# Optimization experiments

Hardware: AMD Instinct MI355X
Metric: run time of the kernel (lower is better)

## Reference

```python
import jax, jax.numpy as jnp
import numpy as np

N_NODES = 50000
N_EDGES = 800000
IN_FEATS, H_FEATS, N_CLASSES = 64, 64, 16


def setup_inputs() -> dict:
    key = jax.random.key(0)
    ks = jax.random.split(key, 8)
    x = jax.random.normal(ks[0], (N_NODES, IN_FEATS), dtype=jnp.float32)
    src = jax.random.randint(ks[1], (N_EDGES,), 0, N_NODES, dtype=jnp.int64)
    dst = jax.random.randint(ks[2], (N_EDGES,), 0, N_NODES, dtype=jnp.int64)
    W_self1 = jax.random.normal(ks[3], (IN_FEATS, H_FEATS), dtype=jnp.float32) / np.sqrt(IN_FEATS)
    W_neigh1 = jax.random.normal(ks[4], (IN_FEATS, H_FEATS), dtype=jnp.float32) / np.sqrt(IN_FEATS)
    b1 = jnp.zeros((H_FEATS,), dtype=jnp.float32)
    W_self2 = jax.random.normal(ks[5], (H_FEATS, N_CLASSES), dtype=jnp.float32) / np.sqrt(H_FEATS)
    W_neigh2 = jax.random.normal(ks[6], (H_FEATS, N_CLASSES), dtype=jnp.float32) / np.sqrt(H_FEATS)
    b2 = jnp.zeros((N_CLASSES,), dtype=jnp.float32)
    return {"x": x, "src": src, "dst": dst,
            "W_self1": W_self1, "W_neigh1": W_neigh1, "b1": b1,
            "W_self2": W_self2, "W_neigh2": W_neigh2, "b2": b2}


def _mean_agg(h, src, dst, n_nodes):
    # gather source-node features along edges, sum into destinations, divide by in-degree
    summed = jax.ops.segment_sum(h[src], dst, num_segments=n_nodes)  # [N, d]
    deg = jax.ops.segment_sum(jnp.ones_like(src, dtype=h.dtype), dst, num_segments=n_nodes)
    return summed / jnp.maximum(deg, 1.0)[:, None]  # zero in-degree -> zeros (DGL semantics)


def _sage_layer(h, src, dst, W_self, W_neigh, b):
    h_neigh = _mean_agg(h, src, dst, h.shape[0])
    return h @ W_self + h_neigh @ W_neigh + b


def reference(x, src, dst, W_self1, W_neigh1, b1, W_self2, W_neigh2, b2):
    h = _sage_layer(x, src, dst, W_self1, W_neigh1, b1)
    h = jax.nn.relu(h)
    out = _sage_layer(h, src, dst, W_self2, W_neigh2, b2)
    return out
```

## Files before the change

### kernel.cpp

```cpp
#include <hip/hip_runtime.h>
#include <hip/hip_bf16.h>
#include <cstring>


#define FEATS 64
#define CLS   16
#define ESCAT 8
#define CAPN  64

typedef unsigned short bf16_t;
typedef float floatx2 __attribute__((ext_vector_type(2)));

__device__ __forceinline__ float bfbits2f(unsigned lo16) {
    unsigned v = lo16 << 16;
    float f;
    __builtin_memcpy(&f, &v, 4);
    return f;
}
__device__ __forceinline__ bf16_t f2bf(float f) {
    unsigned u;
    __builtin_memcpy(&u, &f, 4);
    u = (u + 0x7FFFu + ((u >> 16) & 1u)) >> 16;
    return (bf16_t)u;
}
__device__ __forceinline__ unsigned pack2(float a, float b) {
    return (unsigned)f2bf(a) | ((unsigned)f2bf(b) << 16);
}
__device__ __forceinline__ unsigned pack4_fp8(float a, float b, float c, float d) {
    int q = __builtin_amdgcn_cvt_pk_fp8_f32(a, b, 0, false);
    q = __builtin_amdgcn_cvt_pk_fp8_f32(c, d, q, true);
    return (unsigned)q;
}

__global__ __launch_bounds__(256) void fused_pg_kernel(
    const int* __restrict__ src, const int* __restrict__ dst,
    int* __restrict__ cnt, int* __restrict__ csr, int E,
    const float* __restrict__ x, const float* __restrict__ Ws,
    const float* __restrict__ Wn, bf16_t* __restrict__ selfo,
    unsigned char* __restrict__ t1, int N, int nbp)
{
    __shared__ float smem[16512];
    int t = threadIdx.x;

    if ((int)blockIdx.x < nbp) {
        int e0 = (blockIdx.x * 256 + t) * ESCAT;
#pragma unroll
        for (int h = 0; h < ESCAT / 4; ++h) {
            int e = e0 + h * 4;
            if (e < E) {
                int4 sv = *(const int4*)(src + e);
                int4 dv = *(const int4*)(dst + e);
                int slot;
                slot = atomicAdd(&cnt[dv.x], 1);
                if (slot < CAPN) csr[(size_t)dv.x * CAPN + slot] = sv.x;
                slot = atomicAdd(&cnt[dv.y], 1);
                if (slot < CAPN) csr[(size_t)dv.y * CAPN + slot] = sv.y;
                slot = atomicAdd(&cnt[dv.z], 1);
                if (slot < CAPN) csr[(size_t)dv.z * CAPN + slot] = sv.z;
                slot = atomicAdd(&cnt[dv.w], 1);
                if (slot < CAPN) csr[(size_t)dv.w * CAPN + slot] = sv.w;
            }
        }
        return;
    }

    float* Wc = smem;
    float* xs = smem + 8192;
    int node0 = ((int)blockIdx.x - nbp) * 128;

    for (int idx = t; idx < 64 * 128; idx += 256) {
        int k = idx >> 7, c = idx & 127;
        Wc[idx] = (c < 64) ? Ws[k * 64 + c] : Wn[k * 64 + (c - 64)];
    }
    for (int idx = t; idx < 128 * 16; idx += 256) {
        int row = idx >> 4, c4 = idx & 15;
        int node = node0 + row;
        float4 v = (node < N) ? ((const float4*)(x + (size_t)node * 64))[c4]
                              : make_float4(0.f, 0.f, 0.f, 0.f);
        float* p = &xs[row * 65 + c4 * 4];
        p[0] = v.x; p[1] = v.y; p[2] = v.z; p[3] = v.w;
    }
    __syncthreads();

    int m = t & 31;
    int g = t >> 5;
    float acc[4][16];
#pragma unroll
    for (int j = 0; j < 4; ++j)
#pragma unroll
        for (int c = 0; c < 16; ++c) acc[j][c] = 0.f;

    for (int k = 0; k < 64; ++k) {
        float w[16];
        const float* wp = &Wc[k * 128 + g * 16];
#pragma unroll
        for (int c = 0; c < 16; ++c) w[c] = wp[c];
        float a0 = xs[m * 65 + k];
        float a1 = xs[(m + 32) * 65 + k];
        float a2 = xs[(m + 64) * 65 + k];
        float a3 = xs[(m + 96) * 65 + k];
#pragma unroll
        for (int c = 0; c < 16; ++c) {
            acc[0][c] += a0 * w[c];
            acc[1][c] += a1 * w[c];
            acc[2][c] += a2 * w[c];
            acc[3][c] += a3 * w[c];
        }
    }
#pragma unroll
    for (int j = 0; j < 4; ++j) {
        int node = node0 + m + 32 * j;
        if (node < N) {
            if (g < 4) {
                bf16_t* dstp = selfo + (size_t)node * 64 + g * 16;
                uint4 p0, p1;
                p0.x = pack2(acc[j][0],  acc[j][1]);  p0.y = pack2(acc[j][2],  acc[j][3]);
                p0.z = pack2(acc[j][4],  acc[j][5]);  p0.w = pack2(acc[j][6],  acc[j][7]);
                p1.x = pack2(acc[j][8],  acc[j][9]);  p1.y = pack2(acc[j][10], acc[j][11]);
                p1.z = pack2(acc[j][12], acc[j][13]); p1.w = pack2(acc[j][14], acc[j][15]);
                *(uint4*)(dstp) = p0;
                *(uint4*)(dstp + 8) = p1;
            } else {
                unsigned char* dstp = t1 + (size_t)node * 64 + (g - 4) * 16;
                uint4 q;
                q.x = pack4_fp8(acc[j][0],  acc[j][1],  acc[j][2],  acc[j][3]);
                q.y = pack4_fp8(acc[j][4],  acc[j][5],  acc[j][6],  acc[j][7]);
                q.z = pack4_fp8(acc[j][8],  acc[j][9],  acc[j][10], acc[j][11]);
                q.w = pack4_fp8(acc[j][12], acc[j][13], acc[j][14], acc[j][15]);
                *(uint4*)(dstp) = q;
            }
        }
    }
}

__global__ __launch_bounds__(256) void gather64_kernel(
    const int* __restrict__ csr, const int* __restrict__ cnt,
    const unsigned char* __restrict__ t1, const bf16_t* __restrict__ selfo,
    bf16_t* __restrict__ h1, const float* __restrict__ b1, int N)
{
    int wid = (blockIdx.x * 256 + threadIdx.x) >> 6;
    int lane = threadIdx.x & 63;
    int eslot = lane >> 4;
    int cg = lane & 15;
    if (wid >= N) return;
    int eraw = csr[(size_t)wid * CAPN + lane];
    int d = cnt[wid];
    size_t o = (size_t)wid * 64 + cg * 4;
    uint2 su;
    float4 bb;
    if (eslot == 0) {
        su = *(const uint2*)(selfo + o);
        bb = *(const float4*)(b1 + cg * 4);
    }
    d = min(d, CAPN);
    float ax = 0.f, ay = 0.f, az = 0.f, aw = 0.f;
    if (d > 0) {
        int dm1 = d - 1;
#define G64_ACC(r, m)                                                      \
        {                                                                  \
            floatx2 p_ = __builtin_amdgcn_cvt_pk_f32_fp8((int)(r), false); \
            floatx2 q_ = __builtin_amdgcn_cvt_pk_f32_fp8((int)(r), true);  \
            ax += (m) * p_.x; ay += (m) * p_.y;                            \
            az += (m) * q_.x; aw += (m) * q_.y;                            \
        }
#define G64_BATCH(K0, KN)                                                  \
        {                                                                  \
            int ss[KN - K0];                                               \
            float mk[KN - K0];                                             \
            unsigned rr[KN - K0];                                          \
            _Pragma("unroll")                                              \
            for (int k = K0; k < KN; ++k) {                                \
                int i = eslot + 4 * k;                                     \
                int idx = i > dm1 ? dm1 : i;                               \
                mk[k - K0] = (i <= dm1) ? 1.f : 0.f;                       \
                ss[k - K0] = __shfl(eraw, idx);                            \
            }                                                              \
            _Pragma("unroll")                                              \
            for (int k = 0; k < KN - K0; ++k)                              \
                rr[k] = *(const unsigned*)(t1 + (size_t)ss[k] * 64 + cg * 4); \
            _Pragma("unroll")                                              \
            for (int k = 0; k < KN - K0; ++k) G64_ACC(rr[k], mk[k]);       \
        }
        if (d <= 16) {
            G64_BATCH(0, 4)
        } else if (d <= 32) {
            G64_BATCH(0, 8)
        } else {
            G64_BATCH(0, 16)
        }
#undef G64_BATCH
#undef G64_ACC
        ax += __shfl_xor(ax, 16); ay += __shfl_xor(ay, 16);
        az += __shfl_xor(az, 16); aw += __shfl_xor(aw, 16);
        ax += __shfl_xor(ax, 32); ay += __shfl_xor(ay, 32);
        az += __shfl_xor(az, 32); aw += __shfl_xor(aw, 32);
    }
    if (eslot == 0) {
        float inv = 1.f / fmaxf((float)d, 1.f);
        float rx = fmaxf(bfbits2f(su.x & 0xffff) + ax * inv + bb.x, 0.f);
        float ry = fmaxf(bfbits2f(su.x >> 16)    + ay * inv + bb.y, 0.f);
        float rz = fmaxf(bfbits2f(su.y & 0xffff) + az * inv + bb.z, 0.f);
        float rw = fmaxf(bfbits2f(su.y >> 16)    + aw * inv + bb.w, 0.f);
        uint2 pk;
        pk.x = pack2(rx, ry);
        pk.y = pack2(rz, rw);
        *(uint2*)(h1 + o) = pk;
    }
}

__global__ __launch_bounds__(256) void gather16_kernel(
    const int* __restrict__ csr, const int* __restrict__ cnt,
    const bf16_t* __restrict__ t2,
    float* __restrict__ outp, const float* __restrict__ b2, int N)
{
    int wid = (blockIdx.x * 256 + threadIdx.x) >> 6;
    int lane = threadIdx.x & 63;
    int eslot = lane >> 3;
    int c2 = lane & 7;
    if (wid >= N) return;
    int eraw = csr[(size_t)wid * CAPN + lane];
    int d = cnt[wid];
    size_t o = (size_t)wid * 16 + c2 * 2;
    float2 oo = make_float2(0.f, 0.f), bbv = make_float2(0.f, 0.f);
    if (eslot == 0) {
        oo = *(const float2*)(outp + o);
        bbv = *(const float2*)(b2 + c2 * 2);
    }
    d = min(d, CAPN);
    float a0 = 0.f, a1 = 0.f;
    if (d > 0) {
        int dm1 = d - 1;
#define G16_BATCH(KN)                                                      \
        {                                                                  \
            int ss[KN];                                                    \
            float mk[KN];                                                  \
            unsigned uu[KN];                                               \
            _Pragma("unroll")                                              \
            for (int k = 0; k < KN; ++k) {                                 \
                int i = eslot + 8 * k;                                     \
                int idx = i > dm1 ? dm1 : i;                               \
                mk[k] = (i <= dm1) ? 1.f : 0.f;                            \
                ss[k] = __shfl(eraw, idx);                                 \
            }                                                              \
            _Pragma("unroll")                                              \
            for (int k = 0; k < KN; ++k)                                   \
                uu[k] = *(const unsigned*)(t2 + (size_t)ss[k] * 16 + c2 * 2); \
            _Pragma("unroll")                                              \
            for (int k = 0; k < KN; ++k) {                                 \
                a0 += mk[k] * bfbits2f(uu[k] & 0xffff);                    \
                a1 += mk[k] * bfbits2f(uu[k] >> 16);                       \
            }                                                              \
        }
        if (d <= 16) {
            G16_BATCH(2)
        } else if (d <= 32) {
            G16_BATCH(4)
        } else {
            G16_BATCH(8)
        }
#undef G16_BATCH
        a0 += __shfl_xor(a0, 8);  a1 += __shfl_xor(a1, 8);
        a0 += __shfl_xor(a0, 16); a1 += __shfl_xor(a1, 16);
        a0 += __shfl_xor(a0, 32); a1 += __shfl_xor(a1, 32);
    }
    if (eslot == 0) {
        float inv = 1.f / fmaxf((float)d, 1.f);
        float2 r;
        r.x = oo.x + a0 * inv + bbv.x;
        r.y = oo.y + a1 * inv + bbv.y;
        *(float2*)(outp + o) = r;
    }
}

__global__ __launch_bounds__(256) void gemm2_kernel(
    const bf16_t* __restrict__ h1, const float* __restrict__ Ws,
    const float* __restrict__ Wn, float* __restrict__ outp,
    bf16_t* __restrict__ t2, int N)
{
    __shared__ float Wc[64 * 32];
    __shared__ float xs[128 * 65];
    int t = threadIdx.x;
    int node0 = blockIdx.x * 128;

    for (int idx = t; idx < 64 * 32; idx += 256) {
        int k = idx >> 5, c = idx & 31;
        Wc[idx] = (c < 16) ? Ws[k * 16 + c] : Wn[k * 16 + (c - 16)];
    }
    for (int idx = t; idx < 128 * 8; idx += 256) {
        int row = idx >> 3, c8 = idx & 7;
        int node = node0 + row;
        float* p = &xs[row * 65 + c8 * 8];
        if (node < N) {
            uint4 u = *(const uint4*)(h1 + (size_t)node * 64 + c8 * 8);
            p[0] = bfbits2f(u.x & 0xffff); p[1] = bfbits2f(u.x >> 16);
            p[2] = bfbits2f(u.y & 0xffff); p[3] = bfbits2f(u.y >> 16);
            p[4] = bfbits2f(u.z & 0xffff); p[5] = bfbits2f(u.z >> 16);
            p[6] = bfbits2f(u.w & 0xffff); p[7] = bfbits2f(u.w >> 16);
        } else {
            for (int qq = 0; qq < 8; ++qq) p[qq] = 0.f;
        }
    }
    __syncthreads();

    int m = t & 31;
    int g = t >> 5;
    float acc[4][4];
#pragma unroll
    for (int j = 0; j < 4; ++j)
#pragma unroll
        for (int c = 0; c < 4; ++c) acc[j][c] = 0.f;

    for (int k = 0; k < 64; ++k) {
        float w[4];
        const float* wp = &Wc[k * 32 + g * 4];
#pragma unroll
        for (int c = 0; c < 4; ++c) w[c] = wp[c];
        float a0 = xs[m * 65 + k];
        float a1 = xs[(m + 32) * 65 + k];
        float a2 = xs[(m + 64) * 65 + k];
        float a3 = xs[(m + 96) * 65 + k];
#pragma unroll
        for (int c = 0; c < 4; ++c) {
            acc[0][c] += a0 * w[c];
            acc[1][c] += a1 * w[c];
            acc[2][c] += a2 * w[c];
            acc[3][c] += a3 * w[c];
        }
    }
#pragma unroll
    for (int j = 0; j < 4; ++j) {
        int node = node0 + m + 32 * j;
        if (node < N) {
            if (g < 4) {
                *(float4*)(outp + (size_t)node * 16 + g * 4) =
                    make_float4(acc[j][0], acc[j][1], acc[j][2], acc[j][3]);
            } else {
                uint2 pk;
                pk.x = pack2(acc[j][0], acc[j][1]);
                pk.y = pack2(acc[j][2], acc[j][3]);
                *(uint2*)(t2 + (size_t)node * 16 + (g - 4) * 4) = pk;
            }
        }
    }
}

extern "C" void kernel_launch(void* const* d_in, const int* in_sizes, int n_in,
                              void* d_out, int out_size, void* d_ws, size_t ws_size,
                              hipStream_t stream) {
    const float* x   = (const float*)d_in[0];
    const int*   src = (const int*)d_in[1];
    const int*   dst = (const int*)d_in[2];
    const float* Ws1 = (const float*)d_in[3];
    const float* Wn1 = (const float*)d_in[4];
    const float* b1  = (const float*)d_in[5];
    const float* Ws2 = (const float*)d_in[6];
    const float* Wn2 = (const float*)d_in[7];
    const float* b2  = (const float*)d_in[8];
    float* outp = (float*)d_out;

    const int N = in_sizes[0] / FEATS;
    const int E = in_sizes[1];
    const int NBP = (E + 256 * ESCAT - 1) / (256 * ESCAT);
    const int NBG = (N + 127) / 128;

    char* p = (char*)d_ws;
    auto align16 = [](char* q) { return (char*)(((size_t)q + 15) & ~(size_t)15); };
    int* cnt           = (int*)p;                  p = (char*)(cnt + N);
    int* csr           = (int*)align16(p);         p = (char*)(csr + (size_t)N * CAPN);
    bf16_t* selfo      = (bf16_t*)align16(p);      p = (char*)(selfo + (size_t)N * 64);
    unsigned char* t1  = (unsigned char*)align16(p); p = (char*)(t1 + (size_t)N * 64);
    bf16_t* h1         = (bf16_t*)align16(p);      p = (char*)(h1 + (size_t)N * 64);
    bf16_t* t2         = (bf16_t*)align16(p);

    hipMemsetAsync(cnt, 0, (size_t)N * sizeof(int), stream);

    fused_pg_kernel<<<NBP + NBG, 256, 0, stream>>>(
        src, dst, cnt, csr, E, x, Ws1, Wn1, selfo, t1, N, NBP);

    gather64_kernel<<<((size_t)N * 64 + 255) / 256, 256, 0, stream>>>(
        csr, cnt, t1, selfo, h1, b1, N);
    gemm2_kernel<<<(N + 127) / 128, 256, 0, stream>>>(h1, Ws2, Wn2, outp, t2, N);
    gather16_kernel<<<((size_t)N * 64 + 255) / 256, 256, 0, stream>>>(
        csr, cnt, t2, outp, b2, N);
}
```

Measured before the change: 178.9 us.

## Build CSR via two-pass bucketed partition with shared-memory atomics

Replaces the direct global-atomic scatter into per-node CSR slots with a two-phase scheme. Edges are first partitioned into 256-node buckets using a block-local shared histogram and one global atomic per bucket per block. A new kernel then builds each bucket's CSR rows with shared-memory atomics. This removes heavily contended random global atomics, at the cost of an extra kernel launch and an intermediate edge buffer. It also relies on a fixed bucket capacity (CAP=5120) and on the bucket count fitting in 256.

```diff
diff --git a/kernel.cpp b/kernel.cpp
--- a/kernel.cpp
+++ b/kernel.cpp
@@ -5,7 +5,8 @@
 
 #define FEATS 64
 #define CLS   16
-#define ESCAT 8
+#define EPT   16
+#define CAP   5120
 #define CAPN  64
 
 typedef unsigned short bf16_t;
@@ -34,7 +35,7 @@
 
 __global__ __launch_bounds__(256) void fused_pg_kernel(
     const int* __restrict__ src, const int* __restrict__ dst,
-    int* __restrict__ cnt, int* __restrict__ csr, int E,
+    int* __restrict__ bucket_cnt, int* __restrict__ epart, int E,
     const float* __restrict__ x, const float* __restrict__ Ws,
     const float* __restrict__ Wn, bf16_t* __restrict__ selfo,
     unsigned char* __restrict__ t1, int N, int nbp)
@@ -43,22 +44,33 @@
     int t = threadIdx.x;
 
     if ((int)blockIdx.x < nbp) {
-        int e0 = (blockIdx.x * 256 + t) * ESCAT;
-#pragma unroll
-        for (int h = 0; h < ESCAT / 4; ++h) {
-            int e = e0 + h * 4;
+        int* hist = (int*)smem;
+        int* base = hist + 256;
+        int e0 = blockIdx.x * (256 * EPT);
+        hist[t] = 0;
+        __syncthreads();
+        int pk[EPT];
+        int bk[EPT];
+#pragma unroll
+        for (int j = 0; j < EPT; ++j) {
+            int e = e0 + j * 256 + t;
             if (e < E) {
-                int4 sv = *(const int4*)(src + e);
-                int4 dv = *(const int4*)(dst + e);
-                int slot;
-                slot = atomicAdd(&cnt[dv.x], 1);
-                if (slot < CAPN) csr[(size_t)dv.x * CAPN + slot] = sv.x;
-                slot = atomicAdd(&cnt[dv.y], 1);
-                if (slot < CAPN) csr[(size_t)dv.y * CAPN + slot] = sv.y;
-                slot = atomicAdd(&cnt[dv.z], 1);
-                if (slot < CAPN) csr[(size_t)dv.z * CAPN + slot] = sv.z;
-                slot = atomicAdd(&cnt[dv.w], 1);
-                if (slot < CAPN) csr[(size_t)dv.w * CAPN + slot] = sv.w;
+                int d = dst[e];
+                pk[j] = (src[e] << 8) | (d & 255);
+                bk[j] = d >> 8;
+                atomicAdd(&hist[bk[j]], 1);
+            } else bk[j] = -1;
+        }
+        __syncthreads();
+        int c = hist[t];
+        if (c) base[t] = atomicAdd(&bucket_cnt[t], c);
+        hist[t] = 0;
+        __syncthreads();
+#pragma unroll
+        for (int j = 0; j < EPT; ++j) {
+            if (bk[j] >= 0) {
+                int r = atomicAdd(&hist[bk[j]], 1);
+                epart[bk[j] * CAP + base[bk[j]] + r] = pk[j];
             }
         }
         return;
@@ -133,6 +145,28 @@
     }
 }
 
+__global__ __launch_bounds__(256) void buildcsr_kernel(const int* __restrict__ epart,
+                                                       const int* __restrict__ bucket_cnt,
+                                                       int* __restrict__ cnt,
+                                                       int* __restrict__ csr, int N) {
+    __shared__ int c[256];
+    int t = threadIdx.x;
+    int b = blockIdx.x;
+    int ebeg = b * CAP;
+    int ecnt = bucket_cnt[b];
+    c[t] = 0;
+    __syncthreads();
+    for (int e = t; e < ecnt; e += 256) {
+        int pk = epart[ebeg + e];
+        int ln = pk & 255;
+        int r = atomicAdd(&c[ln], 1);
+        if (r < CAPN) csr[(size_t)(b * 256 + ln) * CAPN + r] = pk >> 8;
+    }
+    __syncthreads();
+    int node = b * 256 + t;
+    if (node < N) cnt[node] = c[t];
+}
+
 __global__ __launch_bounds__(256) void gather64_kernel(
     const int* __restrict__ csr, const int* __restrict__ cnt,
     const unsigned char* __restrict__ t1, const bf16_t* __restrict__ selfo,
@@ -163,30 +197,30 @@
             ax += (m) * p_.x; ay += (m) * p_.y;                            \
             az += (m) * q_.x; aw += (m) * q_.y;                            \
         }
-#define G64_BATCH(K0, KN)                                                  \
+#define G64_BATCH(KN)                                                      \
         {                                                                  \
-            int ss[KN - K0];                                               \
-            float mk[KN - K0];                                             \
-            unsigned rr[KN - K0];                                          \
-            _Pragma("unroll")                                              \
-            for (int k = K0; k < KN; ++k) {                                \
+            int ss[KN];                                                    \
+            float mk[KN];                                                  \
+            unsigned rr[KN];                                               \
+            _Pragma("unroll")                                              \
+            for (int k = 0; k < KN; ++k) {                                 \
                 int i = eslot + 4 * k;                                     \
                 int idx = i > dm1 ? dm1 : i;                               \
-                mk[k - K0] = (i <= dm1) ? 1.f : 0.f;                       \
-                ss[k - K0] = __shfl(eraw, idx);                            \
+                mk[k] = (i <= dm1) ? 1.f : 0.f;                            \
+                ss[k] = __shfl(eraw, idx);                                 \
             }                                                              \
             _Pragma("unroll")                                              \
-            for (int k = 0; k < KN - K0; ++k)                              \
+            for (int k = 0; k < KN; ++k)                                   \
                 rr[k] = *(const unsigned*)(t1 + (size_t)ss[k] * 64 + cg * 4); \
             _Pragma("unroll")                                              \
-            for (int k = 0; k < KN - K0; ++k) G64_ACC(rr[k], mk[k]);       \
+            for (int k = 0; k < KN; ++k) G64_ACC(rr[k], mk[k]);            \
         }
         if (d <= 16) {
-            G64_BATCH(0, 4)
+            G64_BATCH(4)
         } else if (d <= 32) {
-            G64_BATCH(0, 8)
+            G64_BATCH(8)
         } else {
-            G64_BATCH(0, 16)
+            G64_BATCH(16)
         }
 #undef G64_BATCH
 #undef G64_ACC
@@ -360,22 +394,26 @@
 
     const int N = in_sizes[0] / FEATS;
     const int E = in_sizes[1];
-    const int NBP = (E + 256 * ESCAT - 1) / (256 * ESCAT);
+    const int B = (N + 255) / 256;
+    const int NBP = (E + 256 * EPT - 1) / (256 * EPT);
     const int NBG = (N + 127) / 128;
 
     char* p = (char*)d_ws;
     auto align16 = [](char* q) { return (char*)(((size_t)q + 15) & ~(size_t)15); };
-    int* cnt           = (int*)p;                  p = (char*)(cnt + N);
+    int* bucket_cnt    = (int*)p;                  p = (char*)(bucket_cnt + 256);
+    int* epart         = (int*)p;                  p = (char*)(epart + (size_t)B * CAP);
+    int* cnt           = (int*)align16(p);         p = (char*)(cnt + N);
     int* csr           = (int*)align16(p);         p = (char*)(csr + (size_t)N * CAPN);
     bf16_t* selfo      = (bf16_t*)align16(p);      p = (char*)(selfo + (size_t)N * 64);
     unsigned char* t1  = (unsigned char*)align16(p); p = (char*)(t1 + (size_t)N * 64);
     bf16_t* h1         = (bf16_t*)align16(p);      p = (char*)(h1 + (size_t)N * 64);
     bf16_t* t2         = (bf16_t*)align16(p);
 
-    hipMemsetAsync(cnt, 0, (size_t)N * sizeof(int), stream);
+    hipMemsetAsync(bucket_cnt, 0, 256 * sizeof(int), stream);
 
     fused_pg_kernel<<<NBP + NBG, 256, 0, stream>>>(
-        src, dst, cnt, csr, E, x, Ws1, Wn1, selfo, t1, N, NBP);
+        src, dst, bucket_cnt, epart, E, x, Ws1, Wn1, selfo, t1, N, NBP);
+    buildcsr_kernel<<<B, 256, 0, stream>>>(epart, bucket_cnt, cnt, csr, N);
 
     gather64_kernel<<<((size_t)N * 64 + 255) / 256, 256, 0, stream>>>(
         csr, cnt, t1, selfo, h1, b1, N);
```

New measurement: 152.5 us. 1.17x faster.
